# Kernel optimization log

Hardware: AMD Instinct MI355X
Metric: run time of the kernel (lower is better)

The kernel has to match this reference:

```python
import jax, jax.numpy as jnp
import numpy as np

NUM_TASKS = 5
POOL = 5
R = 8
TOPK = 3
SCALE = 1.0  # module self.scale and forward scale arg, both 1
B, S, DIN, DOUT = 4, 4096, 1024, 1024


def setup_inputs() -> dict:
    key = jax.random.key(0)
    ks = jax.random.split(key, 5)
    inp = {
        "input": jax.random.normal(ks[0], (B, S, DIN), dtype=jnp.float32),
        "W": jax.random.normal(ks[1], (DOUT, DIN), dtype=jnp.float32) / np.sqrt(DIN),
        "lora_down": jax.random.normal(ks[2], (POOL, DIN, R), dtype=jnp.float32) / np.sqrt(DIN),
        "lora_up": jax.random.normal(ks[3], (POOL, R, DOUT), dtype=jnp.float32) / np.sqrt(R),
        "lora_route": jax.random.normal(ks[4], (NUM_TASKS, DIN, POOL), dtype=jnp.float32) * 0.02,
        "task_id": 4,
    }
    return inp


def reference(input, W, lora_down, lora_up, lora_route, task_id):
    # Eval branch (self.training == False), 1 <= task_id <= num_tasks.
    task_id = min(task_id, NUM_TASKS)
    k = min(task_id, TOPK)
    route = lora_route[1]                          # [DIN, POOL] (detach split is a no-op for fwd)
    input_mean = jnp.mean(input, axis=1)           # [B, DIN]
    lora_omegas = jnp.mean(input_mean @ route, axis=0)  # [POOL]
    sliced = lora_omegas[1:task_id + 1]            # source slices from 1
    G, I = jax.lax.top_k(sliced, k)                # indices used DIRECTLY (as in source)
    gate = jax.nn.softmax(G)                       # [k]
    # detached expert products (eval path detaches lora_down @ lora_up)
    dw = jax.lax.stop_gradient(
        jnp.einsum('kdr,kro->kdo', lora_down[I], lora_up[I]))  # [k, DIN, DOUT]
    # delta = sum_i gate[i] * SCALE * (input @ dw[i]); forward scale arg = 1
    delta = SCALE * jnp.einsum('k,bsd,kdo->bso', gate, input, dw)
    # delta_w_all[:B//2] = 0
    bmask = (jnp.arange(input.shape[0]) >= input.shape[0] // 2).astype(delta.dtype)
    delta = delta * bmask[:, None, None]
    return input @ W.T + delta
```

## Files before the change

### kernel.cpp

```cpp
#include <hip/hip_runtime.h>
#include <hip/hip_bf16.h>

typedef __attribute__((ext_vector_type(8))) __bf16 bf16x8;
typedef __attribute__((ext_vector_type(4))) __bf16 bf16x4;
typedef __attribute__((ext_vector_type(4))) float f32x4;

#define DIN 1024
#define DOUT 1024
#define MROWS 16384
#define POOLN 5
#define RR 8
#define NTASKS 5
#define TOPKK 3

__device__ __forceinline__ void gemm_tile(const float* __restrict__ A,
                                          const __bf16* __restrict__ Bt,
                                          float* __restrict__ C,
                                          int tm, int tn, int tix,
                                          ushort* lds) {
    const int lane = tix & 63;
    const int wid  = tix >> 6;
    const int wm = wid >> 2, wn = wid & 3;

    const int ar = tix >> 2;
    const int ac = tix & 3;
    const f32x4* __restrict__ pA = (const f32x4*)(A + ((size_t)(tm * 128 + ar)) * 1024 + ac * 8);
    const int awrp  = tix >> 3;
    const int awslot= ((tix & 3) + 4 * ((tix >> 2) & 1)) ^ (awrp & 7);
    const int awoff = awrp * 64 + awslot * 8;

    const int rpl  = lane >> 3;
    const int sl   = (lane & 7) ^ rpl;
    const int srow = rpl * 2 + (sl >> 2);
    const int sc   = sl & 3;
    const char* gB = (const char*)Bt + ((size_t)(tn*256 + wid*32 + srow)) * 2048 + sc * 16;
    const int ldsBst = 4096 + wid * 1024;

    const int rhalf = (lane & 15) >> 1;
    const int slot  = ((lane >> 4) + 4 * (lane & 1)) ^ rhalf;
    const int aoff  = (wm * 32 + rhalf) * 64 + slot * 8;
    const int boff  = 4096 + (wn * 32 + rhalf) * 64 + slot * 8;

    f32x4 acc[4][4];
#pragma unroll
    for (int i = 0; i < 4; ++i)
#pragma unroll
        for (int j = 0; j < 4; ++j) acc[i][j] = (f32x4){0.f, 0.f, 0.f, 0.f};

    auto issueB = [&](int s) {
        const int p = s % 3;
        const size_t kb = (size_t)s * 64;
#pragma unroll
        for (int j = 0; j < 2; ++j) {
            __builtin_amdgcn_global_load_lds(
                (const __attribute__((address_space(1))) void*)(gB + (size_t)j * 32768 + kb),
                (__attribute__((address_space(3))) void*)&lds[p * 12288 + ldsBst + j * 512],
                16, 0, 0);
        }
    };

    auto writeA = [&](int s, f32x4 a0, f32x4 a1) {
        const int p = s % 3;
        bf16x8 v = { (__bf16)a0[0], (__bf16)a0[1], (__bf16)a0[2], (__bf16)a0[3],
                     (__bf16)a1[0], (__bf16)a1[1], (__bf16)a1[2], (__bf16)a1[3] };
        *(bf16x8*)&lds[p * 12288 + awoff] = v;
    };

    auto computeSlab = [&](int s) {
        const int p = s % 3;
        const ushort* aB = &lds[p * 12288 + aoff];
        const ushort* bB = &lds[p * 12288 + boff];
        bf16x8 a[4], b[4];
#pragma unroll
        for (int mi = 0; mi < 4; ++mi) a[mi] = *(const bf16x8*)(aB + mi * 512);
#pragma unroll
        for (int ni = 0; ni < 4; ++ni) b[ni] = *(const bf16x8*)(bB + ni * 512);
        __builtin_amdgcn_s_setprio(1);
#pragma unroll
        for (int mi = 0; mi < 4; ++mi)
#pragma unroll
            for (int ni = 0; ni < 4; ++ni)
                acc[mi][ni] = __builtin_amdgcn_mfma_f32_16x16x32_bf16(
                    a[mi], b[ni], acc[mi][ni], 0, 0, 0);
        __builtin_amdgcn_s_setprio(0);
    };

    f32x4 pa0 = pA[0], pa1 = pA[1];
    issueB(0);
    f32x4 na0 = pA[8], na1 = pA[9];
    issueB(1);
    asm volatile("s_waitcnt vmcnt(6)" ::: "memory");
    writeA(0, pa0, pa1);
    asm volatile("s_waitcnt lgkmcnt(0)" ::: "memory");

#pragma unroll 1
    for (int s = 0; s < 32; ++s) {
        if (s < 31) {
            asm volatile("s_waitcnt vmcnt(2)" ::: "memory");
            writeA(s + 1, na0, na1);
        } else {
            asm volatile("s_waitcnt vmcnt(0)" ::: "memory");
        }
        if (s < 30) {
            na0 = pA[(size_t)(s + 2) * 8];
            na1 = pA[(size_t)(s + 2) * 8 + 1];
            issueB(s + 2);
        }
        __builtin_amdgcn_s_barrier();
        asm volatile("" ::: "memory");
        computeSlab(s);
        asm volatile("" ::: "memory");
        asm volatile("s_waitcnt lgkmcnt(0)" ::: "memory");
        __builtin_amdgcn_s_barrier();
    }

#pragma unroll
    for (int mi = 0; mi < 4; ++mi) {
#pragma unroll
        for (int r = 0; r < 4; ++r) {
            const int grow = tm * 128 + wm * 64 + mi * 16 + (lane >> 4) * 4 + r;
            float* cp = C + (size_t)grow * 1024 + tn * 256 + wn * 64 + (lane & 15);
#pragma unroll
            for (int ni = 0; ni < 4; ++ni) cp[ni * 16] = acc[mi][ni][r];
        }
    }
}

__global__ __launch_bounds__(256) void kW_cvt(const float* __restrict__ W,
                                              __bf16* __restrict__ Wb0) {
    const size_t i = (size_t)(blockIdx.x * 256 + threadIdx.x) * 8;
    f32x4 a = *(const f32x4*)&W[i];
    f32x4 b = *(const f32x4*)&W[i + 4];
    bf16x8 v = { (__bf16)a[0], (__bf16)a[1], (__bf16)a[2], (__bf16)a[3],
                 (__bf16)b[0], (__bf16)b[1], (__bf16)b[2], (__bf16)b[3] };
    *(bf16x8*)&Wb0[i] = v;
}

__global__ __launch_bounds__(512, 4) void k1_mix(const float* __restrict__ in,
                                                 const __bf16* __restrict__ Wb0,
                                                 float* __restrict__ C,
                                                 float* __restrict__ partial) {
    __shared__ ushort lds[36864];
    const int bid = blockIdx.x;
    const int x   = bid & 7;
    const int q   = bid >> 4;
    if (((bid >> 3) & 1) == 0) {
        gemm_tile(in, Wb0, C, x * 8 + (q >> 2), q & 3, threadIdx.x, lds);
        return;
    }
    const int cb = x * 32 + q;
    const int t  = threadIdx.x;
    const int cq = t & 255;
    const int h  = t >> 8;
    const f32x4* __restrict__ base = (const f32x4*)in
        + ((size_t)(cb * 64 + h * 32)) * 256 + cq;
    float s0 = 0.f, s1 = 0.f, s2 = 0.f, s3 = 0.f;
#pragma unroll 1
    for (int j = 0; j < 4; ++j) {
        const f32x4* p = base + (size_t)j * 8 * 256;
        f32x4 v0 = p[0];
        f32x4 v1 = p[256];
        f32x4 v2 = p[512];
        f32x4 v3 = p[768];
        f32x4 v4 = p[1024];
        f32x4 v5 = p[1280];
        f32x4 v6 = p[1536];
        f32x4 v7 = p[1792];
        s0 += v0[0] + v1[0] + v2[0] + v3[0] + v4[0] + v5[0] + v6[0] + v7[0];
        s1 += v0[1] + v1[1] + v2[1] + v3[1] + v4[1] + v5[1] + v6[1] + v7[1];
        s2 += v0[2] + v1[2] + v2[2] + v3[2] + v4[2] + v5[2] + v6[2] + v7[2];
        s3 += v0[3] + v1[3] + v2[3] + v3[3] + v4[3] + v5[3] + v6[3] + v7[3];
    }
    f32x4 pv = { s0, s1, s2, s3 };
    *(f32x4*)&partial[(size_t)(cb * 2 + h) * DIN + cq * 4] = pv;
}

__global__ __launch_bounds__(256) void k1b_reduce(const float* __restrict__ partial,
                                                  float* __restrict__ partial2) {
    const int tid = blockIdx.x * 256 + threadIdx.x;
    const int c = tid & (DIN - 1);
    const int g = tid >> 10;
    float s = 0.f;
    const int r0 = g * 64;
#pragma unroll 8
    for (int r = r0; r < r0 + 64; ++r)
        s += partial[(size_t)r * DIN + c];
    partial2[(size_t)g * DIN + c] = s;
}

__global__ __launch_bounds__(256) void k23b_weights(const float* __restrict__ partial2,
                                                    const float* __restrict__ lroute,
                                                    const int* __restrict__ task_id_p,
                                                    const float* __restrict__ W,
                                                    const float* __restrict__ ldown,
                                                    const float* __restrict__ lup,
                                                    __bf16* __restrict__ Wb1) {
    __shared__ float red[4][POOLN];
    __shared__ float sgate[TOPKK];
    __shared__ int   sgidx[TOPKK];
    const int tix = threadIdx.x;
    const int w = tix >> 6, l = tix & 63;

    float part[POOLN] = {0.f, 0.f, 0.f, 0.f, 0.f};
    {
        const int d0 = tix * 4;
#pragma unroll
        for (int dd = 0; dd < 4; ++dd) {
            const int d = d0 + dd;
            float cs = 0.f;
#pragma unroll
            for (int g = 0; g < 8; ++g) cs += partial2[g * DIN + d];
            cs *= (1.0f / (float)MROWS);
            const float* rp = &lroute[(size_t)1 * DIN * POOLN + (size_t)d * POOLN];
#pragma unroll
            for (int p = 0; p < POOLN; ++p) part[p] += cs * rp[p];
        }
    }
#pragma unroll
    for (int p = 0; p < POOLN; ++p) {
        float v = part[p];
        for (int off = 32; off; off >>= 1) v += __shfl_down(v, off);
        if (l == 0) red[w][p] = v;
    }
    __syncthreads();
    if (tix == 0) {
#pragma unroll
        for (int p = 0; p < POOLN; ++p)
            part[p] = red[0][p] + red[1][p] + red[2][p] + red[3][p];
        int tid = *task_id_p;
        if (tid > NTASKS) tid = NTASKS;
        int L = tid < (POOLN - 1) ? tid : (POOLN - 1);
        int k = tid < TOPKK ? tid : TOPKK;
        float sl[POOLN];
        for (int j = 0; j < L; ++j) sl[j] = part[1 + j];
        float G[TOPKK]; int I[TOPKK];
        int used = 0;
        for (int j = 0; j < k; ++j) {
            int best = -1; float bv = 0.f;
            for (int i2 = 0; i2 < L; ++i2) {
                if (used & (1 << i2)) continue;
                if (best < 0 || sl[i2] > bv) { bv = sl[i2]; best = i2; }
            }
            used |= 1 << best; G[j] = bv; I[j] = best;
        }
        float gt[TOPKK] = {0.f, 0.f, 0.f};
        int   gi[TOPKK] = {0, 0, 0};
        if (k > 0) {
            float m = G[0];
            float e[TOPKK]; float se = 0.f;
            for (int j = 0; j < k; ++j) { e[j] = expf(G[j] - m); se += e[j]; }
            for (int j = 0; j < k; ++j) { gt[j] = e[j] / se; gi[j] = I[j]; }
        }
#pragma unroll
        for (int j = 0; j < TOPKK; ++j) { sgate[j] = gt[j]; sgidx[j] = gi[j]; }
    }
    __syncthreads();

    const int o = blockIdx.x;
    float c[TOPKK][RR];
#pragma unroll
    for (int j = 0; j < TOPKK; ++j) {
        const float g = sgate[j];
        const int   p = sgidx[j];
#pragma unroll
        for (int r = 0; r < RR; ++r)
            c[j][r] = g * lup[(size_t)p * RR * DOUT + (size_t)r * DOUT + o];
    }
    const int d0 = tix * 4;
    const float4 wv = *(const float4*)&W[(size_t)o * DIN + d0];
    float dwv[4] = { 0.f, 0.f, 0.f, 0.f };
#pragma unroll
    for (int j = 0; j < TOPKK; ++j) {
        const int p = sgidx[j];
#pragma unroll
        for (int dd = 0; dd < 4; ++dd) {
            const float4 da = *(const float4*)&ldown[(size_t)p * DIN * RR + (size_t)(d0 + dd) * RR];
            const float4 db = *(const float4*)&ldown[(size_t)p * DIN * RR + (size_t)(d0 + dd) * RR + 4];
            dwv[dd] += da.x * c[j][0] + da.y * c[j][1] + da.z * c[j][2] + da.w * c[j][3]
                     + db.x * c[j][4] + db.y * c[j][5] + db.z * c[j][6] + db.w * c[j][7];
        }
    }
    bf16x4 b1 = { (__bf16)(wv.x + dwv[0]), (__bf16)(wv.y + dwv[1]),
                  (__bf16)(wv.z + dwv[2]), (__bf16)(wv.w + dwv[3]) };
    *(bf16x4*)&Wb1[(size_t)o * DIN + d0] = b1;
}

__global__ __launch_bounds__(512, 4) void k3_gemm(const float* __restrict__ in,
                                                  const __bf16* __restrict__ Wb1,
                                                  float* __restrict__ C) {
    __shared__ ushort lds[36864];
    const int bid = blockIdx.x;
    const int xcd = bid & 7;
    const int idx = bid >> 3;
    gemm_tile(in, Wb1, C, 64 + xcd * 8 + (idx >> 2), idx & 3, threadIdx.x, lds);
}

extern "C" void kernel_launch(void* const* d_in, const int* in_sizes, int n_in,
                              void* d_out, int out_size, void* d_ws, size_t ws_size,
                              hipStream_t stream) {
    const float* in     = (const float*)d_in[0];
    const float* W      = (const float*)d_in[1];
    const float* ldown  = (const float*)d_in[2];
    const float* lup    = (const float*)d_in[3];
    const float* lroute = (const float*)d_in[4];
    const int*   taskid = (const int*)d_in[5];
    float* out = (float*)d_out;

    __bf16* Wb0      = (__bf16*)d_ws;
    __bf16* Wb1      = Wb0 + (size_t)DOUT * DIN;
    float*  partial  = (float*)(Wb1 + (size_t)DOUT * DIN);
    float*  partial2 = partial + 512 * DIN;

    kW_cvt<<<512, 256, 0, stream>>>(W, Wb0);
    k1_mix<<<512, 512, 0, stream>>>(in, Wb0, out, partial);
    k1b_reduce<<<32, 256, 0, stream>>>(partial, partial2);
    k23b_weights<<<1024, 256, 0, stream>>>(partial2, lroute, taskid, W, ldown, lup, Wb1);
    k3_gemm<<<256, 512, 0, stream>>>(in, Wb1, out);
}
```

Before: 103.3 us.

## Apply LoRA delta as low-rank correction after a single base GEMM

Instead of building a merged weight W+dW for the second batch half and running a second GEMM, all rows now go through one base GEMM with W. The second half gets a skinny MFMA projection onto all 40 lora_down columns, and a fix-up kernel adds the gated lora_up contribution into the output. The GEMM pipeline also drops from three LDS stages to two to allow higher occupancy. This removes the dense dW construction and splits routing from the heavy GEMM, but adds a read-modify-write of half the output and shallower prefetching.

New measurement: 355.6 us. +244.1%, slower.

```diff
diff --git a/kernel.cpp b/kernel.cpp
--- a/kernel.cpp
+++ b/kernel.cpp
@@ -4,6 +4,7 @@
 typedef __attribute__((ext_vector_type(8))) __bf16 bf16x8;
 typedef __attribute__((ext_vector_type(4))) __bf16 bf16x4;
 typedef __attribute__((ext_vector_type(4))) float f32x4;
+typedef __attribute__((ext_vector_type(2))) float f32x2;
 
 #define DIN 1024
 #define DOUT 1024
@@ -13,11 +14,11 @@
 #define NTASKS 5
 #define TOPKK 3
 
-__device__ __forceinline__ void gemm_tile(const float* __restrict__ A,
-                                          const __bf16* __restrict__ Bt,
-                                          float* __restrict__ C,
-                                          int tm, int tn, int tix,
-                                          ushort* lds) {
+__device__ __forceinline__ void gemm_tile_d1(const float* __restrict__ A,
+                                             const __bf16* __restrict__ Bt,
+                                             float* __restrict__ C,
+                                             int tm, int tn, int tix,
+                                             ushort* lds) {
     const int lane = tix & 63;
     const int wid  = tix >> 6;
     const int wm = wid >> 2, wn = wid & 3;
@@ -48,7 +49,7 @@
         for (int j = 0; j < 4; ++j) acc[i][j] = (f32x4){0.f, 0.f, 0.f, 0.f};
 
     auto issueB = [&](int s) {
-        const int p = s % 3;
+        const int p = s & 1;
         const size_t kb = (size_t)s * 64;
 #pragma unroll
         for (int j = 0; j < 2; ++j) {
@@ -58,16 +59,14 @@
                 16, 0, 0);
         }
     };
-
     auto writeA = [&](int s, f32x4 a0, f32x4 a1) {
-        const int p = s % 3;
+        const int p = s & 1;
         bf16x8 v = { (__bf16)a0[0], (__bf16)a0[1], (__bf16)a0[2], (__bf16)a0[3],
                      (__bf16)a1[0], (__bf16)a1[1], (__bf16)a1[2], (__bf16)a1[3] };
         *(bf16x8*)&lds[p * 12288 + awoff] = v;
     };
-
     auto computeSlab = [&](int s) {
-        const int p = s % 3;
+        const int p = s & 1;
         const ushort* aB = &lds[p * 12288 + aoff];
         const ushort* bB = &lds[p * 12288 + boff];
         bf16x8 a[4], b[4];
@@ -101,17 +100,17 @@
         } else {
             asm volatile("s_waitcnt vmcnt(0)" ::: "memory");
         }
-        if (s < 30) {
-            na0 = pA[(size_t)(s + 2) * 8];
-            na1 = pA[(size_t)(s + 2) * 8 + 1];
-            issueB(s + 2);
-        }
         __builtin_amdgcn_s_barrier();
         asm volatile("" ::: "memory");
         computeSlab(s);
         asm volatile("" ::: "memory");
         asm volatile("s_waitcnt lgkmcnt(0)" ::: "memory");
         __builtin_amdgcn_s_barrier();
+        if (s < 30) {
+            na0 = pA[(size_t)(s + 2) * 8];
+            na1 = pA[(size_t)(s + 2) * 8 + 1];
+            issueB(s + 2);
+        }
     }
 
 #pragma unroll
@@ -127,52 +126,97 @@
 }
 
 __global__ __launch_bounds__(256) void kW_cvt(const float* __restrict__ W,
-                                              __bf16* __restrict__ Wb0) {
-    const size_t i = (size_t)(blockIdx.x * 256 + threadIdx.x) * 8;
+                                              const float* __restrict__ ldown,
+                                              __bf16* __restrict__ Wb0,
+                                              __bf16* __restrict__ DT5) {
+    const int tid = blockIdx.x * 256 + threadIdx.x;
+    const size_t i = (size_t)tid * 8;
     f32x4 a = *(const f32x4*)&W[i];
     f32x4 b = *(const f32x4*)&W[i + 4];
     bf16x8 v = { (__bf16)a[0], (__bf16)a[1], (__bf16)a[2], (__bf16)a[3],
                  (__bf16)b[0], (__bf16)b[1], (__bf16)b[2], (__bf16)b[3] };
     *(bf16x8*)&Wb0[i] = v;
-}
-
-__global__ __launch_bounds__(512, 4) void k1_mix(const float* __restrict__ in,
-                                                 const __bf16* __restrict__ Wb0,
-                                                 float* __restrict__ C,
-                                                 float* __restrict__ partial) {
-    __shared__ ushort lds[36864];
+    if (tid < 49152) {
+        const int j = tid >> 10;
+        const int d = tid & 1023;
+        float val = 0.f;
+        if (j < 40) val = ldown[(size_t)(j >> 3) * 8192 + d * 8 + (j & 7)];
+        DT5[(size_t)j * 1024 + d] = (__bf16)val;
+    }
+}
+
+__global__ __launch_bounds__(512, 6) void kMain(const float* __restrict__ in,
+                                                const __bf16* __restrict__ Wb0,
+                                                const __bf16* __restrict__ DT5,
+                                                float* __restrict__ C,
+                                                float* __restrict__ partial,
+                                                float* __restrict__ Pws) {
+    __shared__ ushort lds[24576];
     const int bid = blockIdx.x;
-    const int x   = bid & 7;
-    const int q   = bid >> 4;
-    if (((bid >> 3) & 1) == 0) {
-        gemm_tile(in, Wb0, C, x * 8 + (q >> 2), q & 3, threadIdx.x, lds);
+    if (bid < 512) {
+        const int xcd = bid & 7;
+        const int idx = bid >> 3;
+        gemm_tile_d1(in, Wb0, C, xcd * 16 + (idx >> 2), idx & 3, threadIdx.x, lds);
         return;
     }
-    const int cb = x * 32 + q;
+    if (bid < 768) {
+        const int cb = bid - 512;
+        const int t  = threadIdx.x;
+        const int cq = t & 255;
+        const int h  = t >> 8;
+        const f32x4* __restrict__ base = (const f32x4*)in
+            + ((size_t)(cb * 64 + h * 32)) * 256 + cq;
+        float s0 = 0.f, s1 = 0.f, s2 = 0.f, s3 = 0.f;
+#pragma unroll 1
+        for (int j = 0; j < 4; ++j) {
+            const f32x4* p = base + (size_t)j * 8 * 256;
+            f32x4 v0 = p[0];
+            f32x4 v1 = p[256];
+            f32x4 v2 = p[512];
+            f32x4 v3 = p[768];
+            f32x4 v4 = p[1024];
+            f32x4 v5 = p[1280];
+            f32x4 v6 = p[1536];
+            f32x4 v7 = p[1792];
+            s0 += v0[0] + v1[0] + v2[0] + v3[0] + v4[0] + v5[0] + v6[0] + v7[0];
+            s1 += v0[1] + v1[1] + v2[1] + v3[1] + v4[1] + v5[1] + v6[1] + v7[1];
+            s2 += v0[2] + v1[2] + v2[2] + v3[2] + v4[2] + v5[2] + v6[2] + v7[2];
+            s3 += v0[3] + v1[3] + v2[3] + v3[3] + v4[3] + v5[3] + v6[3] + v7[3];
+        }
+        f32x4 pv = { s0, s1, s2, s3 };
+        *(f32x4*)&partial[(size_t)(cb * 2 + h) * DIN + cq * 4] = pv;
+        return;
+    }
+    const int pb = bid - 768;
     const int t  = threadIdx.x;
-    const int cq = t & 255;
-    const int h  = t >> 8;
-    const f32x4* __restrict__ base = (const f32x4*)in
-        + ((size_t)(cb * 64 + h * 32)) * 256 + cq;
-    float s0 = 0.f, s1 = 0.f, s2 = 0.f, s3 = 0.f;
+    const int lane = t & 63;
+    const int w = t >> 6;
+    const int row = 8192 + pb * 128 + w * 16 + (lane & 15);
+    const int kb  = (lane >> 4) * 8;
+    const float* inr = in + (size_t)row * 1024;
+    f32x4 acc[3];
+#pragma unroll
+    for (int nf = 0; nf < 3; ++nf) acc[nf] = (f32x4){0.f, 0.f, 0.f, 0.f};
 #pragma unroll 1
-    for (int j = 0; j < 4; ++j) {
-        const f32x4* p = base + (size_t)j * 8 * 256;
-        f32x4 v0 = p[0];
-        f32x4 v1 = p[256];
-        f32x4 v2 = p[512];
-        f32x4 v3 = p[768];
-        f32x4 v4 = p[1024];
-        f32x4 v5 = p[1280];
-        f32x4 v6 = p[1536];
-        f32x4 v7 = p[1792];
-        s0 += v0[0] + v1[0] + v2[0] + v3[0] + v4[0] + v5[0] + v6[0] + v7[0];
-        s1 += v0[1] + v1[1] + v2[1] + v3[1] + v4[1] + v5[1] + v6[1] + v7[1];
-        s2 += v0[2] + v1[2] + v2[2] + v3[2] + v4[2] + v5[2] + v6[2] + v7[2];
-        s3 += v0[3] + v1[3] + v2[3] + v3[3] + v4[3] + v5[3] + v6[3] + v7[3];
-    }
-    f32x4 pv = { s0, s1, s2, s3 };
-    *(f32x4*)&partial[(size_t)(cb * 2 + h) * DIN + cq * 4] = pv;
+    for (int ks = 0; ks < 32; ++ks) {
+        const int k0 = ks * 32 + kb;
+        f32x4 a0 = *(const f32x4*)&inr[k0];
+        f32x4 a1 = *(const f32x4*)&inr[k0 + 4];
+        bf16x8 af = { (__bf16)a0[0], (__bf16)a0[1], (__bf16)a0[2], (__bf16)a0[3],
+                      (__bf16)a1[0], (__bf16)a1[1], (__bf16)a1[2], (__bf16)a1[3] };
+#pragma unroll
+        for (int nf = 0; nf < 3; ++nf) {
+            bf16x8 bf = *(const bf16x8*)&DT5[(size_t)(nf * 16 + (lane & 15)) * 1024 + k0];
+            acc[nf] = __builtin_amdgcn_mfma_f32_16x16x32_bf16(af, bf, acc[nf], 0, 0, 0);
+        }
+    }
+#pragma unroll
+    for (int nf = 0; nf < 3; ++nf)
+#pragma unroll
+        for (int r = 0; r < 4; ++r) {
+            const int prow = pb * 128 + w * 16 + (lane >> 4) * 4 + r;
+            Pws[(size_t)prow * 48 + nf * 16 + (lane & 15)] = acc[nf][r];
+        }
 }
 
 __global__ __launch_bounds__(256) void k1b_reduce(const float* __restrict__ partial,
@@ -188,22 +232,23 @@
     partial2[(size_t)g * DIN + c] = s;
 }
 
-__global__ __launch_bounds__(256) void k23b_weights(const float* __restrict__ partial2,
-                                                    const float* __restrict__ lroute,
-                                                    const int* __restrict__ task_id_p,
-                                                    const float* __restrict__ W,
-                                                    const float* __restrict__ ldown,
-                                                    const float* __restrict__ lup,
-                                                    __bf16* __restrict__ Wb1) {
+__global__ __launch_bounds__(512) void kFix(const float* __restrict__ partial2,
+                                            const float* __restrict__ lroute,
+                                            const int* __restrict__ task_id_p,
+                                            const float* __restrict__ lup,
+                                            const float* __restrict__ Pws,
+                                            float* __restrict__ C) {
     __shared__ float red[4][POOLN];
     __shared__ float sgate[TOPKK];
     __shared__ int   sgidx[TOPKK];
-    const int tix = threadIdx.x;
-    const int w = tix >> 6, l = tix & 63;
-
-    float part[POOLN] = {0.f, 0.f, 0.f, 0.f, 0.f};
-    {
-        const int d0 = tix * 4;
+    __shared__ float Pl[16][48];
+    const int t = threadIdx.x;
+    const int blk = blockIdx.x;
+
+    if (t < 256) {
+        const int w = t >> 6, l = t & 63;
+        float part[POOLN] = {0.f, 0.f, 0.f, 0.f, 0.f};
+        const int d0 = t * 4;
 #pragma unroll
         for (int dd = 0; dd < 4; ++dd) {
             const int d = d0 + dd;
@@ -215,15 +260,16 @@
 #pragma unroll
             for (int p = 0; p < POOLN; ++p) part[p] += cs * rp[p];
         }
-    }
-#pragma unroll
-    for (int p = 0; p < POOLN; ++p) {
-        float v = part[p];
-        for (int off = 32; off; off >>= 1) v += __shfl_down(v, off);
-        if (l == 0) red[w][p] = v;
+#pragma unroll
+        for (int p = 0; p < POOLN; ++p) {
+            float v = part[p];
+            for (int off = 32; off; off >>= 1) v += __shfl_down(v, off);
+            if (l == 0) red[w][p] = v;
+        }
     }
     __syncthreads();
-    if (tix == 0) {
+    if (t == 0) {
+        float part[POOLN];
 #pragma unroll
         for (int p = 0; p < POOLN; ++p)
             part[p] = red[0][p] + red[1][p] + red[2][p] + red[3][p];
@@ -254,45 +300,42 @@
 #pragma unroll
         for (int j = 0; j < TOPKK; ++j) { sgate[j] = gt[j]; sgidx[j] = gi[j]; }
     }
+    if (t < 192) {
+        const int r = t / 12, cq = t % 12;
+        f32x4 v = *(const f32x4*)&Pws[(size_t)(blk * 16 + r) * 48 + cq * 4];
+        *(f32x4*)&Pl[r][cq * 4] = v;
+    }
     __syncthreads();
 
-    const int o = blockIdx.x;
-    float c[TOPKK][RR];
-#pragma unroll
-    for (int j = 0; j < TOPKK; ++j) {
-        const float g = sgate[j];
-        const int   p = sgidx[j];
-#pragma unroll
-        for (int r = 0; r < RR; ++r)
-            c[j][r] = g * lup[(size_t)p * RR * DOUT + (size_t)r * DOUT + o];
-    }
-    const int d0 = tix * 4;
-    const float4 wv = *(const float4*)&W[(size_t)o * DIN + d0];
-    float dwv[4] = { 0.f, 0.f, 0.f, 0.f };
-#pragma unroll
-    for (int j = 0; j < TOPKK; ++j) {
-        const int p = sgidx[j];
-#pragma unroll
-        for (int dd = 0; dd < 4; ++dd) {
-            const float4 da = *(const float4*)&ldown[(size_t)p * DIN * RR + (size_t)(d0 + dd) * RR];
-            const float4 db = *(const float4*)&ldown[(size_t)p * DIN * RR + (size_t)(d0 + dd) * RR + 4];
-            dwv[dd] += da.x * c[j][0] + da.y * c[j][1] + da.z * c[j][2] + da.w * c[j][3]
-                     + db.x * c[j][4] + db.y * c[j][5] + db.z * c[j][6] + db.w * c[j][7];
-        }
-    }
-    bf16x4 b1 = { (__bf16)(wv.x + dwv[0]), (__bf16)(wv.y + dwv[1]),
-                  (__bf16)(wv.z + dwv[2]), (__bf16)(wv.w + dwv[3]) };
-    *(bf16x4*)&Wb1[(size_t)o * DIN + d0] = b1;
-}
-
-__global__ __launch_bounds__(512, 4) void k3_gemm(const float* __restrict__ in,
-                                                  const __bf16* __restrict__ Wb1,
-                                                  float* __restrict__ C) {
-    __shared__ ushort lds[36864];
-    const int bid = blockIdx.x;
-    const int xcd = bid & 7;
-    const int idx = bid >> 3;
-    gemm_tile(in, Wb1, C, 64 + xcd * 8 + (idx >> 2), idx & 3, threadIdx.x, lds);
+    const int n0 = t * 2;
+    float ug[24][2];
+    int pcol[24];
+#pragma unroll
+    for (int k = 0; k < TOPKK; ++k) {
+        const float g = sgate[k];
+        const int   p = sgidx[k];
+#pragma unroll
+        for (int r = 0; r < RR; ++r) {
+            const float* u = &lup[(size_t)p * RR * DOUT + (size_t)r * DOUT + n0];
+            ug[k * 8 + r][0] = g * u[0];
+            ug[k * 8 + r][1] = g * u[1];
+            pcol[k * 8 + r] = p * 8 + r;
+        }
+    }
+#pragma unroll 1
+    for (int m = 0; m < 16; ++m) {
+        float a0 = 0.f, a1 = 0.f;
+#pragma unroll
+        for (int j = 0; j < 24; ++j) {
+            const float pv = Pl[m][pcol[j]];
+            a0 += pv * ug[j][0];
+            a1 += pv * ug[j][1];
+        }
+        float* cp = C + (size_t)(8192 + blk * 16 + m) * 1024 + n0;
+        f32x2 cv = *(f32x2*)cp;
+        cv[0] += a0; cv[1] += a1;
+        *(f32x2*)cp = cv;
+    }
 }
 
 extern "C" void kernel_launch(void* const* d_in, const int* in_sizes, int n_in,
@@ -307,13 +350,13 @@
     float* out = (float*)d_out;
 
     __bf16* Wb0      = (__bf16*)d_ws;
-    __bf16* Wb1      = Wb0 + (size_t)DOUT * DIN;
-    float*  partial  = (float*)(Wb1 + (size_t)DOUT * DIN);
+    __bf16* DT5      = Wb0 + (size_t)DOUT * DIN;
+    float*  partial  = (float*)(DT5 + 48 * 1024);
     float*  partial2 = partial + 512 * DIN;
-
-    kW_cvt<<<512, 256, 0, stream>>>(W, Wb0);
-    k1_mix<<<512, 512, 0, stream>>>(in, Wb0, out, partial);
+    float*  Pws      = partial2 + 8 * DIN;
+
+    kW_cvt<<<512, 256, 0, stream>>>(W, ldown, Wb0, DT5);
+    kMain<<<832, 512, 0, stream>>>(in, Wb0, DT5, out, partial, Pws);
     k1b_reduce<<<32, 256, 0, stream>>>(partial, partial2);
-    k23b_weights<<<1024, 256, 0, stream>>>(partial2, lroute, taskid, W, ldown, lup, Wb1);
-    k3_gemm<<<256, 512, 0, stream>>>(in, Wb1, out);
-}
+    kFix<<<512, 512, 0, stream>>>(partial2, lroute, taskid, lup, Pws, out);
+}
```
